# Optimization experiments

Hardware: AMD Instinct MI355X
Metric: run time of the kernel (lower is better)

## Reference

```python
import jax, jax.numpy as jnp
import numpy as np

B, T, M, P = 64, 2048, 512, 512


def setup_inputs() -> dict:
    key = jax.random.key(0)
    ks = jax.random.split(key, 9)
    s = 0.02
    return {
        "hidden_state": jax.random.normal(ks[0], (B, P), jnp.float32),
        "cell_state": jax.random.normal(ks[1], (B, P), jnp.float32),
        "encoder_h": jax.random.normal(ks[2], (B, T, M), jnp.float32),
        # Dense W_d: (2p -> m)
        "W_d": jax.random.normal(ks[3], (2 * P, M), jnp.float32) * s,
        "b_wd": jnp.zeros((M,), jnp.float32),
        # Dense U_d: (m -> m)
        "U_d": jax.random.normal(ks[4], (M, M), jnp.float32) * s,
        "b_ud": jnp.zeros((M,), jnp.float32),
        # Dense v_d: (m -> 1)
        "v_d": jax.random.normal(ks[5], (M, 1), jnp.float32) * s,
        "b_vd": jnp.zeros((1,), jnp.float32),
    }


def reference(hidden_state, cell_state, encoder_h, W_d, b_wd, U_d, b_ud, v_d, b_vd):
    # W_d(RepeatVector(T)(concat([d, s]))): the Dense is applied to the same
    # (B, 2p) vector at every time step, so compute it once and broadcast.
    ds = jnp.concatenate([hidden_state, cell_state], axis=-1)          # (B, 2p)
    ds_proj = ds @ W_d + b_wd                                          # (B, m)
    enc_proj = jnp.einsum('btm,mn->btn', encoder_h, U_d) + b_ud        # (B, T, m)
    e = jnp.tanh(ds_proj[:, None, :] + enc_proj)                       # (B, T, m)
    l = e @ v_d + b_vd                                                 # (B, T, 1)
    return jax.nn.softmax(l, axis=1)                                   # softmax over T
```

## Files before the change

kernel.cpp:

```cpp
#include <hip/hip_runtime.h>
#include <cstdint>
#include <cstddef>


typedef float  floatx4 __attribute__((ext_vector_type(4)));
typedef short  shortx8 __attribute__((ext_vector_type(8)));
typedef unsigned int uintx4 __attribute__((ext_vector_type(4)));

__device__ __forceinline__ short f2bf_rne(float f) {
  unsigned u = __float_as_uint(f);
  unsigned r = u + 0x7FFFu + ((u >> 16) & 1u);
  return (short)(r >> 16);
}

__device__ __forceinline__ unsigned pack_bf_trunc(float lo, float hi) {
  return __builtin_amdgcn_perm(__float_as_uint(hi), __float_as_uint(lo), 0x07060302u);
}

#define SB() __builtin_amdgcn_sched_barrier(0)
#define WAIT_VM0() asm volatile("s_waitcnt vmcnt(0)" ::: "memory")
#define WAIT_VM8() asm volatile("s_waitcnt vmcnt(8)" ::: "memory")
#define WAIT_LGKM0() asm volatile("s_waitcnt lgkmcnt(0)" ::: "memory")
#define BAR() __builtin_amdgcn_s_barrier()

extern "C" __global__ __launch_bounds__(256) void prep_kernel(
    const float* __restrict__ hidden, const float* __restrict__ cell,
    const float* __restrict__ W_d, const float* __restrict__ b_wd,
    const float* __restrict__ U_d, const float* __restrict__ b_ud,
    float* __restrict__ S, short* __restrict__ UT, float* __restrict__ lzero)
{
  int bx = blockIdx.x, tid = threadIdx.x;
  if (bx < 128) {
    int idx = bx * 256 + tid;
    int b = idx >> 9, n = idx & 511;
    const float* h = hidden + b * 512;
    const float* c = cell   + b * 512;
    float a0 = b_wd[n] + b_ud[n], a1 = 0.f, a2 = 0.f, a3 = 0.f;
    for (int k = 0; k < 512; k += 4) {
      a0 = fmaf(h[k + 0], W_d[(k + 0) * 512 + n], a0);
      a1 = fmaf(h[k + 1], W_d[(k + 1) * 512 + n], a1);
      a2 = fmaf(h[k + 2], W_d[(k + 2) * 512 + n], a2);
      a3 = fmaf(h[k + 3], W_d[(k + 3) * 512 + n], a3);
    }
    for (int k = 0; k < 512; k += 4) {
      a0 = fmaf(c[k + 0], W_d[(k + 512) * 512 + n], a0);
      a1 = fmaf(c[k + 1], W_d[(k + 513) * 512 + n], a1);
      a2 = fmaf(c[k + 2], W_d[(k + 514) * 512 + n], a2);
      a3 = fmaf(c[k + 3], W_d[(k + 515) * 512 + n], a3);
    }
    S[idx] = (a0 + a1) + (a2 + a3);
  } else if (bx < 384) {
    int idx = (bx - 128) * 1024 + tid * 4;
    int n = idx >> 9, k0 = idx & 511;
    unsigned lo = (unsigned short)f2bf_rne(U_d[(size_t)(k0 + 0) * 512 + n]) |
                  ((unsigned)(unsigned short)f2bf_rne(U_d[(size_t)(k0 + 1) * 512 + n]) << 16);
    unsigned hi = (unsigned short)f2bf_rne(U_d[(size_t)(k0 + 2) * 512 + n]) |
                  ((unsigned)(unsigned short)f2bf_rne(U_d[(size_t)(k0 + 3) * 512 + n]) << 16);
    uint2 w; w.x = lo; w.y = hi;
    *(uint2*)(UT + idx) = w;
  } else {
    int idx = ((bx - 384) * 256 + tid) * 4;
    floatx4 z = {0.f, 0.f, 0.f, 0.f};
    *(floatx4*)(lzero + idx) = z;
  }
}

struct GemmState {
  short (*As)[8192];
  const float* aptr;
  const short* bfp[4];
  int afrag0, awbase;
};

template <int T>
__device__ __forceinline__ void kiter(
    GemmState& st, shortx8 (&bfr)[2][4][2], floatx4 (&areg)[8],
    floatx4 (&acc)[8][4])
{
  constexpr int CUR = T & 1;
  constexpr int NXT = CUR ^ 1;
  const short* Ab = &st.As[CUR][0];
  shortx8 af[4][2];

#pragma unroll
  for (int tr = 0; tr < 4; ++tr)
#pragma unroll
    for (int s = 0; s < 2; ++s)
      af[tr][s] = *(const shortx8*)(Ab + ((st.afrag0 + tr * 1024) ^ (s * 32)));
  SB();
  if constexpr (T < 7) {
#pragma unroll
    for (int tc = 0; tc < 4; ++tc)
#pragma unroll
      for (int s = 0; s < 2; ++s)
        bfr[NXT][tc][s] = *(const shortx8*)(st.bfp[tc] + (T + 1) * 64 + s * 32);
  }
  SB();
  WAIT_LGKM0(); SB();
  __builtin_amdgcn_s_setprio(1);
#pragma unroll
  for (int tr = 0; tr < 4; ++tr)
#pragma unroll
    for (int tc = 0; tc < 4; ++tc)
#pragma unroll
      for (int s = 0; s < 2; ++s)
        acc[tr][tc] = __builtin_amdgcn_mfma_f32_16x16x32_bf16(
            af[tr][s], bfr[CUR][tc][s], acc[tr][tc], 0, 0, 0);
  __builtin_amdgcn_s_setprio(0);
  SB(); BAR(); SB();

  if constexpr (T < 7) {
    WAIT_VM8(); SB();
    short* An = &st.As[NXT][0];
#pragma unroll
    for (int gi = 0; gi < 4; ++gi) {
      uintx4 w;
      w.x = pack_bf_trunc(areg[2 * gi].x, areg[2 * gi].y);
      w.y = pack_bf_trunc(areg[2 * gi].z, areg[2 * gi].w);
      w.z = pack_bf_trunc(areg[2 * gi + 1].x, areg[2 * gi + 1].y);
      w.w = pack_bf_trunc(areg[2 * gi + 1].z, areg[2 * gi + 1].w);
      *(uintx4*)(An + (st.awbase ^ (gi * 8))) = w;
    }
    SB();
  }
#pragma unroll
  for (int tr = 0; tr < 4; ++tr)
#pragma unroll
    for (int s = 0; s < 2; ++s)
      af[tr][s] = *(const shortx8*)(Ab + ((st.afrag0 + (tr + 4) * 1024) ^ (s * 32)));
  SB();
  if constexpr (T < 6) {
#pragma unroll
    for (int i = 0; i < 8; ++i)
      areg[i] = *(const floatx4*)(st.aptr + (T + 2) * 64 + i * 4);
  }
  SB();
  WAIT_LGKM0(); SB();
  __builtin_amdgcn_s_setprio(1);
#pragma unroll
  for (int tr = 0; tr < 4; ++tr)
#pragma unroll
    for (int tc = 0; tc < 4; ++tc)
#pragma unroll
      for (int s = 0; s < 2; ++s)
        acc[tr + 4][tc] = __builtin_amdgcn_mfma_f32_16x16x32_bf16(
            af[tr][s], bfr[CUR][tc][s], acc[tr + 4][tc], 0, 0, 0);
  __builtin_amdgcn_s_setprio(0);
  SB();
  if constexpr (T < 7) {
    if constexpr (T < 6) { WAIT_VM8(); }
    else                 { WAIT_VM0(); }
    SB(); BAR(); SB();
  }
}

extern "C" __global__ __launch_bounds__(256, 2) void attn_gemm(
    const float* __restrict__ A, const short* __restrict__ UT,
    const float* __restrict__ S, const float* __restrict__ vd,
    float* __restrict__ lout)
{
  __shared__ short As[2][8192];

  const int tid = threadIdx.x;
  const int bx  = blockIdx.x;
  const int xcd = bx & 7;
  const int wg  = xcd * 256 + (bx >> 3);
  const int cb  = wg & 1;
  const int rb  = wg >> 1;
  const int row0 = rb << 7;
  const int col0 = cb << 8;
  const int wave = tid >> 6;
  const int lane = tid & 63;
  const int wc = wave;
  const int q = lane >> 4, l15 = lane & 15;

  GemmState st;
  st.As = As;

  const int arow = tid >> 1;
  const int ah   = tid & 1;
  st.aptr   = A + (size_t)(row0 + arow) * 512 + ah * 32;
  st.awbase = arow * 64 + ((((ah * 4) ^ (arow & 7)) & 7) << 3);

#pragma unroll
  for (int tc = 0; tc < 4; ++tc)
    st.bfp[tc] = UT + (size_t)(col0 + wc * 64 + tc * 16 + l15) * 512 + q * 8;

  st.afrag0 = l15 * 64 + ((q ^ (l15 & 7)) << 3);

  floatx4 acc[8][4];
#pragma unroll
  for (int i = 0; i < 8; ++i)
#pragma unroll
    for (int j = 0; j < 4; ++j)
      acc[i][j] = (floatx4){0.f, 0.f, 0.f, 0.f};

  floatx4 areg[8];
  shortx8 bfr[2][4][2];

  SB();
#pragma unroll
  for (int i = 0; i < 8; ++i) areg[i] = *(const floatx4*)(st.aptr + i * 4);
  SB();
#pragma unroll
  for (int tc = 0; tc < 4; ++tc)
#pragma unroll
    for (int s = 0; s < 2; ++s)
      bfr[0][tc][s] = *(const shortx8*)(st.bfp[tc] + s * 32);
  SB();
  WAIT_VM8(); SB();
#pragma unroll
  for (int gi = 0; gi < 4; ++gi) {
    uintx4 w;
    w.x = pack_bf_trunc(areg[2 * gi].x, areg[2 * gi].y);
    w.y = pack_bf_trunc(areg[2 * gi].z, areg[2 * gi].w);
    w.z = pack_bf_trunc(areg[2 * gi + 1].x, areg[2 * gi + 1].y);
    w.w = pack_bf_trunc(areg[2 * gi + 1].z, areg[2 * gi + 1].w);
    *(uintx4*)(&As[0][st.awbase ^ (gi * 8)]) = w;
  }
  SB();
#pragma unroll
  for (int i = 0; i < 8; ++i) areg[i] = *(const floatx4*)(st.aptr + 64 + i * 4);
  SB();
  WAIT_VM8(); SB();
  WAIT_LGKM0(); SB();
  BAR(); SB();

  kiter<0>(st, bfr, areg, acc);
  kiter<1>(st, bfr, areg, acc);
  kiter<2>(st, bfr, areg, acc);
  kiter<3>(st, bfr, areg, acc);
  kiter<4>(st, bfr, areg, acc);
  kiter<5>(st, bfr, areg, acc);
  kiter<6>(st, bfr, areg, acc);
  kiter<7>(st, bfr, areg, acc);

  const int bb = rb >> 4;
  const float* Srow = S + bb * 512;
  float sv[4], vv[4];
#pragma unroll
  for (int tc = 0; tc < 4; ++tc) {
    int n = col0 + wc * 64 + tc * 16 + l15;
    sv[tc] = Srow[n];
    vv[tc] = vd[n];
  }
#pragma unroll
  for (int tr = 0; tr < 8; ++tr) {
#pragma unroll
    for (int r = 0; r < 4; ++r) {
      float ssum = 0.f;
#pragma unroll
      for (int tc = 0; tc < 4; ++tc) {
        float x = acc[tr][tc][r] + sv[tc];
        x = fminf(15.f, fmaxf(-15.f, x));
        float e2 = __expf(2.f * x);
        float e = (e2 - 1.f) / (e2 + 1.f);
        ssum += e * vv[tc];
      }
      ssum += __shfl_xor(ssum, 1);
      ssum += __shfl_xor(ssum, 2);
      ssum += __shfl_xor(ssum, 4);
      ssum += __shfl_xor(ssum, 8);
      if (l15 == 0) {
        int row = row0 + tr * 16 + q * 4 + r;
        atomicAdd(lout + row, ssum);
      }
    }
  }
}

extern "C" __global__ __launch_bounds__(256) void softmax_t(float* __restrict__ l)
{
  int b = blockIdx.x, tid = threadIdx.x;
  int wave = tid >> 6, lane = tid & 63;
  float* row = l + (size_t)b * 2048;
  float v[8];
  float mx = -3.4e38f;
#pragma unroll
  for (int i = 0; i < 8; ++i) { v[i] = row[tid + i * 256]; mx = fmaxf(mx, v[i]); }
#pragma unroll
  for (int m = 1; m < 64; m <<= 1) mx = fmaxf(mx, __shfl_xor(mx, m));
  __shared__ float red[8];
  if (lane == 0) red[wave] = mx;
  __syncthreads();
  mx = fmaxf(fmaxf(red[0], red[1]), fmaxf(red[2], red[3]));
  float s = 0.f;
#pragma unroll
  for (int i = 0; i < 8; ++i) { v[i] = __expf(v[i] - mx); s += v[i]; }
#pragma unroll
  for (int m = 1; m < 64; m <<= 1) s += __shfl_xor(s, m);
  if (lane == 0) red[4 + wave] = s;
  __syncthreads();
  s = red[4] + red[5] + red[6] + red[7];
  float inv = 1.f / s;
#pragma unroll
  for (int i = 0; i < 8; ++i) row[tid + i * 256] = v[i] * inv;
}

extern "C" void kernel_launch(void* const* d_in, const int* in_sizes, int n_in,
                              void* d_out, int out_size, void* d_ws, size_t ws_size,
                              hipStream_t stream) {
  const float* hidden = (const float*)d_in[0];
  const float* cell   = (const float*)d_in[1];
  const float* enc    = (const float*)d_in[2];
  const float* W_d    = (const float*)d_in[3];
  const float* b_wd   = (const float*)d_in[4];
  const float* U_d    = (const float*)d_in[5];
  const float* b_ud   = (const float*)d_in[6];
  const float* v_d    = (const float*)d_in[7];
  float* out = (float*)d_out;
  float* S   = (float*)d_ws;
  short* UT  = (short*)((char*)d_ws + 32768 * sizeof(float));

  hipLaunchKernelGGL(prep_kernel, dim3(512), dim3(256), 0, stream,
                     hidden, cell, W_d, b_wd, U_d, b_ud, S, UT, out);
  hipLaunchKernelGGL(attn_gemm, dim3(2048), dim3(256), 0, stream,
                     enc, UT, S, v_d, out);
  hipLaunchKernelGGL(softmax_t, dim3(64), dim3(256), 0, stream, out);
}
```

Measured before the change: 574.4 us.

## Halve GEMM row tile to 64 rows and merge per-iteration barriers

```diff
diff --git a/kernel.cpp b/kernel.cpp
--- a/kernel.cpp
+++ b/kernel.cpp
@@ -19,6 +19,7 @@
 
 #define SB() __builtin_amdgcn_sched_barrier(0)
 #define WAIT_VM0() asm volatile("s_waitcnt vmcnt(0)" ::: "memory")
+#define WAIT_VM4() asm volatile("s_waitcnt vmcnt(4)" ::: "memory")
 #define WAIT_VM8() asm volatile("s_waitcnt vmcnt(8)" ::: "memory")
 #define WAIT_LGKM0() asm volatile("s_waitcnt lgkmcnt(0)" ::: "memory")
 #define BAR() __builtin_amdgcn_s_barrier()
@@ -66,7 +67,7 @@
 }
 
 struct GemmState {
-  short (*As)[8192];
+  short (*As)[4096];
   const float* aptr;
   const short* bfp[4];
   int afrag0, awbase;
@@ -74,8 +75,8 @@
 
 template <int T>
 __device__ __forceinline__ void kiter(
-    GemmState& st, shortx8 (&bfr)[2][4][2], floatx4 (&areg)[8],
-    floatx4 (&acc)[8][4])
+    GemmState& st, shortx8 (&bfr)[2][4][2], floatx4 (&areg)[4],
+    floatx4 (&acc)[4][4])
 {
   constexpr int CUR = T & 1;
   constexpr int NXT = CUR ^ 1;
@@ -99,7 +100,7 @@
   WAIT_LGKM0(); SB();
   __builtin_amdgcn_s_setprio(1);
 #pragma unroll
-  for (int tr = 0; tr < 4; ++tr)
+  for (int tr = 0; tr < 2; ++tr)
 #pragma unroll
     for (int tc = 0; tc < 4; ++tc)
 #pragma unroll
@@ -107,50 +108,46 @@
         acc[tr][tc] = __builtin_amdgcn_mfma_f32_16x16x32_bf16(
             af[tr][s], bfr[CUR][tc][s], acc[tr][tc], 0, 0, 0);
   __builtin_amdgcn_s_setprio(0);
-  SB(); BAR(); SB();
-
+  SB();
   if constexpr (T < 7) {
     WAIT_VM8(); SB();
     short* An = &st.As[NXT][0];
-#pragma unroll
-    for (int gi = 0; gi < 4; ++gi) {
-      uintx4 w;
-      w.x = pack_bf_trunc(areg[2 * gi].x, areg[2 * gi].y);
-      w.y = pack_bf_trunc(areg[2 * gi].z, areg[2 * gi].w);
-      w.z = pack_bf_trunc(areg[2 * gi + 1].x, areg[2 * gi + 1].y);
-      w.w = pack_bf_trunc(areg[2 * gi + 1].z, areg[2 * gi + 1].w);
-      *(uintx4*)(An + (st.awbase ^ (gi * 8))) = w;
-    }
+    uintx4 w0, w1;
+    w0.x = pack_bf_trunc(areg[0].x, areg[0].y);
+    w0.y = pack_bf_trunc(areg[0].z, areg[0].w);
+    w0.z = pack_bf_trunc(areg[1].x, areg[1].y);
+    w0.w = pack_bf_trunc(areg[1].z, areg[1].w);
+    w1.x = pack_bf_trunc(areg[2].x, areg[2].y);
+    w1.y = pack_bf_trunc(areg[2].z, areg[2].w);
+    w1.z = pack_bf_trunc(areg[3].x, areg[3].y);
+    w1.w = pack_bf_trunc(areg[3].z, areg[3].w);
+    *(uintx4*)(An + st.awbase)       = w0;
+    *(uintx4*)(An + (st.awbase ^ 8)) = w1;
     SB();
   }
-#pragma unroll
-  for (int tr = 0; tr < 4; ++tr)
-#pragma unroll
-    for (int s = 0; s < 2; ++s)
-      af[tr][s] = *(const shortx8*)(Ab + ((st.afrag0 + (tr + 4) * 1024) ^ (s * 32)));
-  SB();
   if constexpr (T < 6) {
 #pragma unroll
-    for (int i = 0; i < 8; ++i)
+    for (int i = 0; i < 4; ++i)
       areg[i] = *(const floatx4*)(st.aptr + (T + 2) * 64 + i * 4);
   }
   SB();
-  WAIT_LGKM0(); SB();
   __builtin_amdgcn_s_setprio(1);
 #pragma unroll
-  for (int tr = 0; tr < 4; ++tr)
+  for (int tr = 2; tr < 4; ++tr)
 #pragma unroll
     for (int tc = 0; tc < 4; ++tc)
 #pragma unroll
       for (int s = 0; s < 2; ++s)
-        acc[tr + 4][tc] = __builtin_amdgcn_mfma_f32_16x16x32_bf16(
-            af[tr][s], bfr[CUR][tc][s], acc[tr + 4][tc], 0, 0, 0);
+        acc[tr][tc] = __builtin_amdgcn_mfma_f32_16x16x32_bf16(
+            af[tr][s], bfr[CUR][tc][s], acc[tr][tc], 0, 0, 0);
   __builtin_amdgcn_s_setprio(0);
   SB();
   if constexpr (T < 7) {
-    if constexpr (T < 6) { WAIT_VM8(); }
+    if constexpr (T < 6) { WAIT_VM4(); }
     else                 { WAIT_VM0(); }
-    SB(); BAR(); SB();
+    SB();
+    WAIT_LGKM0(); SB();
+    BAR(); SB();
   }
 }
 
@@ -159,28 +156,27 @@
     const float* __restrict__ S, const float* __restrict__ vd,
     float* __restrict__ lout)
 {
-  __shared__ short As[2][8192];
+  __shared__ short As[2][4096];
 
   const int tid = threadIdx.x;
   const int bx  = blockIdx.x;
   const int xcd = bx & 7;
-  const int wg  = xcd * 256 + (bx >> 3);
+  const int wg  = xcd * 512 + (bx >> 3);
   const int cb  = wg & 1;
   const int rb  = wg >> 1;
-  const int row0 = rb << 7;
+  const int row0 = rb << 6;
   const int col0 = cb << 8;
-  const int wave = tid >> 6;
   const int lane = tid & 63;
-  const int wc = wave;
+  const int wc = tid >> 6;
   const int q = lane >> 4, l15 = lane & 15;
 
   GemmState st;
   st.As = As;
 
-  const int arow = tid >> 1;
-  const int ah   = tid & 1;
-  st.aptr   = A + (size_t)(row0 + arow) * 512 + ah * 32;
-  st.awbase = arow * 64 + ((((ah * 4) ^ (arow & 7)) & 7) << 3);
+  const int arow = tid >> 2;
+  const int akq  = tid & 3;
+  st.aptr   = A + (size_t)(row0 + arow) * 512 + akq * 16;
+  st.awbase = arow * 64 + (((2 * akq) ^ (arow & 7)) << 3);
 
 #pragma unroll
   for (int tc = 0; tc < 4; ++tc)
@@ -188,19 +184,19 @@
 
   st.afrag0 = l15 * 64 + ((q ^ (l15 & 7)) << 3);
 
-  floatx4 acc[8][4];
-#pragma unroll
-  for (int i = 0; i < 8; ++i)
+  floatx4 acc[4][4];
+#pragma unroll
+  for (int i = 0; i < 4; ++i)
 #pragma unroll
     for (int j = 0; j < 4; ++j)
       acc[i][j] = (floatx4){0.f, 0.f, 0.f, 0.f};
 
-  floatx4 areg[8];
+  floatx4 areg[4];
   shortx8 bfr[2][4][2];
 
   SB();
 #pragma unroll
-  for (int i = 0; i < 8; ++i) areg[i] = *(const floatx4*)(st.aptr + i * 4);
+  for (int i = 0; i < 4; ++i) areg[i] = *(const floatx4*)(st.aptr + i * 4);
   SB();
 #pragma unroll
   for (int tc = 0; tc < 4; ++tc)
@@ -209,20 +205,24 @@
       bfr[0][tc][s] = *(const shortx8*)(st.bfp[tc] + s * 32);
   SB();
   WAIT_VM8(); SB();
-#pragma unroll
-  for (int gi = 0; gi < 4; ++gi) {
-    uintx4 w;
-    w.x = pack_bf_trunc(areg[2 * gi].x, areg[2 * gi].y);
-    w.y = pack_bf_trunc(areg[2 * gi].z, areg[2 * gi].w);
-    w.z = pack_bf_trunc(areg[2 * gi + 1].x, areg[2 * gi + 1].y);
-    w.w = pack_bf_trunc(areg[2 * gi + 1].z, areg[2 * gi + 1].w);
-    *(uintx4*)(&As[0][st.awbase ^ (gi * 8)]) = w;
-  }
-  SB();
-#pragma unroll
-  for (int i = 0; i < 8; ++i) areg[i] = *(const floatx4*)(st.aptr + 64 + i * 4);
-  SB();
-  WAIT_VM8(); SB();
+  {
+    uintx4 w0, w1;
+    w0.x = pack_bf_trunc(areg[0].x, areg[0].y);
+    w0.y = pack_bf_trunc(areg[0].z, areg[0].w);
+    w0.z = pack_bf_trunc(areg[1].x, areg[1].y);
+    w0.w = pack_bf_trunc(areg[1].z, areg[1].w);
+    w1.x = pack_bf_trunc(areg[2].x, areg[2].y);
+    w1.y = pack_bf_trunc(areg[2].z, areg[2].w);
+    w1.z = pack_bf_trunc(areg[3].x, areg[3].y);
+    w1.w = pack_bf_trunc(areg[3].z, areg[3].w);
+    *(uintx4*)(&As[0][st.awbase])       = w0;
+    *(uintx4*)(&As[0][st.awbase ^ 8])   = w1;
+  }
+  SB();
+#pragma unroll
+  for (int i = 0; i < 4; ++i) areg[i] = *(const floatx4*)(st.aptr + 64 + i * 4);
+  SB();
+  WAIT_VM4(); SB();
   WAIT_LGKM0(); SB();
   BAR(); SB();
 
@@ -235,7 +235,7 @@
   kiter<6>(st, bfr, areg, acc);
   kiter<7>(st, bfr, areg, acc);
 
-  const int bb = rb >> 4;
+  const int bb = rb >> 5;
   const float* Srow = S + bb * 512;
   float sv[4], vv[4];
 #pragma unroll
@@ -245,7 +245,7 @@
     vv[tc] = vd[n];
   }
 #pragma unroll
-  for (int tr = 0; tr < 8; ++tr) {
+  for (int tr = 0; tr < 4; ++tr) {
 #pragma unroll
     for (int r = 0; r < 4; ++r) {
       float ssum = 0.f;
@@ -314,7 +314,7 @@
 
   hipLaunchKernelGGL(prep_kernel, dim3(512), dim3(256), 0, stream,
                      hidden, cell, W_d, b_wd, U_d, b_ud, S, UT, out);
-  hipLaunchKernelGGL(attn_gemm, dim3(2048), dim3(256), 0, stream,
+  hipLaunchKernelGGL(attn_gemm, dim3(4096), dim3(256), 0, stream,
                      enc, UT, S, v_d, out);
   hipLaunchKernelGGL(softmax_t, dim3(64), dim3(256), 0, stream, out);
 }
```

Measured after the change: 502.4 us. 12.5% less time.
